# Kernel optimization log

Hardware: AMD Instinct MI355X
Metric: run time of the kernel (lower is better)

The kernel has to match this reference:

```python
import jax, jax.numpy as jnp
import numpy as np

D_MODEL = 1024
N_HEADS = 16
SEQ = 2048
BATCH = 2


def setup_inputs() -> dict:
    key = jax.random.key(0)
    ks = jax.random.split(key, 12)
    s = 1.0 / np.sqrt(D_MODEL)
    return {
        "q_input": jax.random.normal(ks[0], (BATCH, SEQ, D_MODEL), jnp.float32),
        "k_input": jax.random.normal(ks[1], (BATCH, SEQ, D_MODEL), jnp.float32),
        "v_input": jax.random.normal(ks[2], (BATCH, SEQ, D_MODEL), jnp.float32),
        "key_padding_mask": jnp.zeros((BATCH, SEQ), dtype=bool),
        "wq": jax.random.normal(ks[3], (D_MODEL, D_MODEL), jnp.float32) * s,
        "bq": jnp.zeros((D_MODEL,), jnp.float32),
        "wk": jax.random.normal(ks[4], (D_MODEL, D_MODEL), jnp.float32) * s,
        "bk": jnp.zeros((D_MODEL,), jnp.float32),
        "wv": jax.random.normal(ks[5], (D_MODEL, D_MODEL), jnp.float32) * s,
        "bv": jnp.zeros((D_MODEL,), jnp.float32),
        "wo": jax.random.normal(ks[6], (D_MODEL, D_MODEL), jnp.float32) * s,
        "bo": jnp.zeros((D_MODEL,), jnp.float32),
    }


def reference(q_input, k_input, v_input, key_padding_mask, wq, bq, wk, bk, wv, bv, wo, bo):
    B, Lq, _ = q_input.shape
    Lk = k_input.shape[1]
    d_head = D_MODEL // N_HEADS
    # torch Linear: x @ W.T + b
    Q = q_input @ wq.T + bq
    K = k_input @ wk.T + bk
    V = v_input @ wv.T + bv
    # [B, H, L, d_head]
    Qh = Q.reshape(B, Lq, N_HEADS, d_head).transpose(0, 2, 1, 3)
    Kh = K.reshape(B, Lk, N_HEADS, d_head).transpose(0, 2, 1, 3)
    Vh = V.reshape(B, Lk, N_HEADS, d_head).transpose(0, 2, 1, 3)
    scores = jnp.einsum("bhqd,bhkd->bhqk", Qh, Kh) / jnp.sqrt(jnp.float32(d_head))
    # causal mask (use_mask=True)
    causal = jnp.arange(Lk)[None, :] > jnp.arange(Lq)[:, None]  # [Lq, Lk]
    scores = jnp.where(causal[None, None], -jnp.inf, scores)
    # key padding mask [B,1,1,Lk]
    scores = jnp.where(key_padding_mask[:, None, None, :], -jnp.inf, scores)
    # module's global all-inf fallback (scalar condition)
    probs = jnp.where(
        jnp.all(jnp.isinf(scores)),
        jnp.full_like(scores, 1.0 / Lk),
        jax.nn.softmax(scores, axis=-1),
    )
    # dropout is identity in eval mode
    out = jnp.einsum("bhqk,bhkd->bhqd", probs, Vh)
    out = out.transpose(0, 2, 1, 3).reshape(B, Lq, D_MODEL)
    return out @ wo.T + bo
```

## Files before the change

### kernel.cpp

```cpp
#include <hip/hip_runtime.h>
#include <cstdint>
#include <cstddef>

#define DM   1024
#define HEADS 16
#define DH    64
#define SEQL  2048
#define BATCH 2
#define MTOT  (BATCH*SEQL)

typedef __attribute__((ext_vector_type(8))) short short8;
typedef __attribute__((ext_vector_type(4))) float floatx4;

__device__ __forceinline__ unsigned short f2bf(float f) {
  unsigned int u = __float_as_uint(f);
  u = (u + 0x7FFFu + ((u >> 16) & 1u)) >> 16;
  return (unsigned short)u;
}

__device__ __forceinline__ float exp2_fast(float x) {
#if __has_builtin(__builtin_amdgcn_exp2f)
  return __builtin_amdgcn_exp2f(x);
#else
  return exp2f(x);
#endif
}

__device__ __forceinline__ unsigned int cvt_pk_bf16(float lo, float hi) {
  unsigned int r;
  asm("v_cvt_pk_bf16_f32 %0, %1, %2" : "=v"(r) : "v"(lo), "v"(hi));
  return r;
}

__device__ __forceinline__ void async_ld16(const void* g, void* l) {
  __builtin_amdgcn_global_load_lds(
      (const __attribute__((address_space(1))) unsigned int*)g,
      (__attribute__((address_space(3))) unsigned int*)l, 16, 0, 0);
}

#define QSCALE 0.1803368801111204f

__global__ void cvt_all(const float* __restrict__ q, const float* __restrict__ k,
                        const float* __restrict__ v, const float* __restrict__ w0,
                        const float* __restrict__ w1, const float* __restrict__ w2,
                        const float* __restrict__ w3,
                        unsigned short* __restrict__ Xq, unsigned short* __restrict__ Xk,
                        unsigned short* __restrict__ Xv, unsigned short* __restrict__ W0,
                        unsigned short* __restrict__ W1, unsigned short* __restrict__ W2,
                        unsigned short* __restrict__ W3) {
  const int bid = blockIdx.x;
  const float* src; unsigned short* dst; int base;
  if (bid < 12288) {
    int seg = bid >> 12;
    base = (bid & 4095) * 1024;
    src = seg == 0 ? q : seg == 1 ? k : v;
    dst = seg == 0 ? Xq : seg == 1 ? Xk : Xv;
  } else {
    int b2 = bid - 12288;
    int seg = b2 >> 10;
    base = (b2 & 1023) * 1024;
    src = seg == 0 ? w0 : seg == 1 ? w1 : seg == 2 ? w2 : w3;
    dst = seg == 0 ? W0 : seg == 1 ? W1 : seg == 2 ? W2 : W3;
  }
  int i = base + threadIdx.x * 4;
  float4 vv = *(const float4*)(src + i);
  ushort4 o;
  o.x = f2bf(vv.x); o.y = f2bf(vv.y); o.z = f2bf(vv.z); o.w = f2bf(vv.w);
  *(ushort4*)(dst + i) = o;
}

__global__ __launch_bounds__(256, 3) void qkv_gemm(
    const unsigned short* Xq, const unsigned short* Xk, const unsigned short* Xv,
    const unsigned short* Wq, const unsigned short* Wk, const unsigned short* Wv,
    const float* bq, const float* bk, const float* bv,
    unsigned short* Qo, unsigned short* Ko, unsigned short* VTo) {
  __shared__ unsigned short As[128 * 64], Bs[128 * 64];
  const unsigned short *A, *Bw; const float* bias; unsigned short* Cout;
  if (blockIdx.z == 0)      { A = Xq; Bw = Wq; bias = bq; Cout = Qo; }
  else if (blockIdx.z == 1) { A = Xk; Bw = Wk; bias = bk; Cout = Ko; }
  else                      { A = Xv; Bw = Wv; bias = bv; Cout = VTo; }

  const int K = DM, N = DM;
  const int m0 = blockIdx.y * 128, n0 = blockIdx.x * 128;
  const int tid  = threadIdx.x;
  const int lane = tid & 63, wvi = tid >> 6;
  const int lq = lane & 15, quad = lane >> 4;
  const int wrow = wvi >> 1, wcol = wvi & 1;

  floatx4 acc[4][4];
  #pragma unroll
  for (int i = 0; i < 4; i++)
    #pragma unroll
    for (int j = 0; j < 4; j++)
      #pragma unroll
      for (int e = 0; e < 4; e++) acc[i][j][e] = 0.0f;

  for (int kt = 0; kt < K; kt += 64) {
    #pragma unroll
    for (int cc = 0; cc < 4; cc++) {
      int c = wvi + cc * 4;
      int e = c * 512 + lane * 8;
      int r = e >> 6, col = e & 63;
      async_ld16(A  + (size_t)(m0 + r) * K + kt + col, As + c * 512);
      async_ld16(Bw + (size_t)(n0 + r) * K + kt + col, Bs + c * 512);
    }
    __syncthreads();
    #pragma unroll
    for (int ks = 0; ks < 64; ks += 32) {
      short8 af[4], bf[4];
      #pragma unroll
      for (int i = 0; i < 4; i++)
        af[i] = *(const short8*)&As[(wrow * 64 + i * 16 + lq) * 64 + ks + quad * 8];
      #pragma unroll
      for (int j = 0; j < 4; j++)
        bf[j] = *(const short8*)&Bs[(wcol * 64 + j * 16 + lq) * 64 + ks + quad * 8];
      #pragma unroll
      for (int i = 0; i < 4; i++)
        #pragma unroll
        for (int j = 0; j < 4; j++)
          acc[i][j] = __builtin_amdgcn_mfma_f32_16x16x32_bf16(af[i], bf[j], acc[i][j], 0, 0, 0);
    }
    __syncthreads();
  }

  if (blockIdx.z == 2) {
    #pragma unroll
    for (int i = 0; i < 4; i++) {
      const int rowg = m0 + wrow * 64 + i * 16 + quad * 4;
      const int bb  = rowg >> 11;
      const int kt2 = (rowg & 2047) >> 6;
      const int k0  = rowg & 63;
      #pragma unroll
      for (int j = 0; j < 4; j++) {
        const int colg = n0 + wcol * 64 + j * 16 + lq;
        const int h2 = colg >> 6, d2 = colg & 63;
        const float bb_v = bias[colg];
        ushort4 w;
        w.x = f2bf(acc[i][j][0] + bb_v);
        w.y = f2bf(acc[i][j][1] + bb_v);
        w.z = f2bf(acc[i][j][2] + bb_v);
        w.w = f2bf(acc[i][j][3] + bb_v);
        *(ushort4*)(Cout + (size_t)((bb * HEADS + h2) * 32 + kt2) * 4096 + d2 * 64 + k0) = w;
      }
    }
  } else {
    const float oscale = (blockIdx.z == 0) ? QSCALE : 1.0f;
    #pragma unroll
    for (int i = 0; i < 4; i++) {
      #pragma unroll
      for (int j = 0; j < 4; j++) {
        int colg = n0 + wcol * 64 + j * 16 + lq;
        float bb = bias[colg];
        #pragma unroll
        for (int r = 0; r < 4; r++) {
          int rowg = m0 + wrow * 64 + i * 16 + quad * 4 + r;
          Cout[(size_t)rowg * N + colg] = f2bf((acc[i][j][r] + bb) * oscale);
        }
      }
    }
  }
}

__global__ __launch_bounds__(256, 4) void out_gemm(
    const unsigned short* __restrict__ A, const unsigned short* __restrict__ Bw,
    const float* __restrict__ bias, float* __restrict__ C) {
  __shared__ unsigned short As[64 * 64], Bs[128 * 64];
  const int K = DM, N = DM;
  const int m0 = blockIdx.y * 64, n0 = blockIdx.x * 128;
  const int tid  = threadIdx.x;
  const int lane = tid & 63, wvi = tid >> 6;
  const int lq = lane & 15, quad = lane >> 4;

  floatx4 acc[8];
  #pragma unroll
  for (int j = 0; j < 8; j++)
    #pragma unroll
    for (int e = 0; e < 4; e++) acc[j][e] = 0.0f;

  for (int kt = 0; kt < K; kt += 64) {
    #pragma unroll
    for (int cc = 0; cc < 2; cc++) {
      int c = wvi + cc * 4;
      int e = c * 512 + lane * 8;
      int r = e >> 6, col = e & 63;
      async_ld16(A + (size_t)(m0 + r) * K + kt + col, As + c * 512);
    }
    #pragma unroll
    for (int cc = 0; cc < 4; cc++) {
      int c = wvi + cc * 4;
      int e = c * 512 + lane * 8;
      int r = e >> 6, col = e & 63;
      async_ld16(Bw + (size_t)(n0 + r) * K + kt + col, Bs + c * 512);
    }
    __syncthreads();
    #pragma unroll
    for (int ks = 0; ks < 64; ks += 32) {
      const short8 af = *(const short8*)&As[(wvi * 16 + lq) * 64 + ks + quad * 8];
      #pragma unroll
      for (int j = 0; j < 8; j++) {
        const short8 bf = *(const short8*)&Bs[(j * 16 + lq) * 64 + ks + quad * 8];
        acc[j] = __builtin_amdgcn_mfma_f32_16x16x32_bf16(af, bf, acc[j], 0, 0, 0);
      }
    }
    __syncthreads();
  }

  #pragma unroll
  for (int j = 0; j < 8; j++) {
    const int colg = n0 + j * 16 + lq;
    const float bb = bias[colg];
    #pragma unroll
    for (int r = 0; r < 4; r++) {
      const int rowg = m0 + wvi * 16 + quad * 4 + r;
      C[(size_t)rowg * N + colg] = acc[j][r] + bb;
    }
  }
}

__global__ __launch_bounds__(256, 2) void attn_kernel(
    const unsigned short* __restrict__ Q, const unsigned short* __restrict__ K,
    const unsigned short* __restrict__ VT, const unsigned char* __restrict__ kpm,
    unsigned short* __restrict__ O) {
  __shared__ unsigned short Ks[64 * 72];
  __shared__ unsigned short VTs[64 * 72];
  __shared__ unsigned short Ps[4][2][16 * 72];

  const int bid = blockIdx.x;
  const int qt = 15 - (bid >> 5);
  const int bh = bid & 31;
  const int h = bh & 15, b = bh >> 4;
  const int tid = threadIdx.x, lane = tid & 63, wvi = tid >> 6;
  const int lq = lane & 15, quad = lane >> 4;
  const size_t bbase = (size_t)b * SEQL * DM;

  const int srow = tid >> 4;
  const int scol = (tid & 15) * 4;

  const unsigned short* kptr = K + bbase + (size_t)h * DH + (size_t)srow * DM + scol;
  const unsigned short* vptr = VT + (size_t)(b * HEADS + h) * 32 * 4096 + srow * 64 + scol;
  const unsigned char*  mptr = kpm + (size_t)b * SEQL + quad * 4;

  short8 qf[2][2];
  #pragma unroll
  for (int g = 0; g < 2; g++) {
    const unsigned short* Qrow =
        Q + bbase + (size_t)(qt * 128 + g * 64 + wvi * 16 + lq) * DM + h * DH;
    qf[g][0] = *(const short8*)(Qrow + quad * 8);
    qf[g][1] = *(const short8*)(Qrow + 32 + quad * 8);
  }

  ushort4 kr[4], vr[4];
  unsigned int mr[4];
  #pragma unroll
  for (int j = 0; j < 4; j++) {
    kr[j] = *(const ushort4*)(kptr + (size_t)j * 16 * DM);
    vr[j] = *(const ushort4*)(vptr + j * 1024);
  }
  #pragma unroll
  for (int t = 0; t < 4; t++) mr[t] = *(const unsigned int*)(mptr + t * 16);
  kptr += (size_t)64 * DM; vptr += 4096; mptr += 64;

  floatx4 o[2][4];
  floatx4 lacc[2];
  #pragma unroll
  for (int g = 0; g < 2; g++) {
    #pragma unroll
    for (int t = 0; t < 4; t++)
      #pragma unroll
      for (int e = 0; e < 4; e++) o[g][t][e] = 0.f;
    #pragma unroll
    for (int e = 0; e < 4; e++) lacc[g][e] = 0.f;
  }

  floatx4 zf;
  #pragma unroll
  for (int e = 0; e < 4; e++) zf[e] = 0.f;

  short8 ones8;
  #pragma unroll
  for (int e = 0; e < 8; e++) ones8[e] = (short)0x3F80;

  const int qg = wvi * 16 + lq;

  auto tile_body = [&](int m0, int m1, const unsigned int* mcur) {
    floatx4 st[2][4];
    #pragma unroll
    for (int t = 0; t < 4; t++) {
      const short8 a0 = *(const short8*)&Ks[(t * 16 + lq) * 72 + quad * 8];
      const short8 a1 = *(const short8*)&Ks[(t * 16 + lq) * 72 + 32 + quad * 8];
      if (m0 != 2) {
        st[0][t] = __builtin_amdgcn_mfma_f32_16x16x32_bf16(a0, qf[0][0], zf, 0, 0, 0);
        st[0][t] = __builtin_amdgcn_mfma_f32_16x16x32_bf16(a1, qf[0][1], st[0][t], 0, 0, 0);
      }
      st[1][t] = __builtin_amdgcn_mfma_f32_16x16x32_bf16(a0, qf[1][0], zf, 0, 0, 0);
      st[1][t] = __builtin_amdgcn_mfma_f32_16x16x32_bf16(a1, qf[1][1], st[1][t], 0, 0, 0);
    }

    const bool any_pad =
        __any((int)((mcur[0] | mcur[1] | mcur[2] | mcur[3]) != 0u));

    #pragma unroll
    for (int g = 0; g < 2; g++) {
      if (g == 0 && m0 == 2) continue;
      const int dmode = (g == 0) ? m0 : m1;
      float x[4][4];
      #pragma unroll
      for (int t = 0; t < 4; t++)
        #pragma unroll
        for (int r = 0; r < 4; r++) x[t][r] = st[g][t][r];

      if (any_pad) {
        #pragma unroll
        for (int t = 0; t < 4; t++)
          #pragma unroll
          for (int r = 0; r < 4; r++)
            if ((mcur[t] >> (8 * r)) & 0xffu) x[t][r] = -1e33f;
      }
      if (dmode == 1) {
        #pragma unroll
        for (int t = 0; t < 4; t++)
          #pragma unroll
          for (int r = 0; r < 4; r++)
            if (t * 16 + quad * 4 + r > qg) x[t][r] = -1e33f;
      }

      #pragma unroll
      for (int t = 0; t < 4; t++)
        #pragma unroll
        for (int r = 0; r < 4; r++)
          x[t][r] = exp2_fast(x[t][r]);

      #pragma unroll
      for (int t = 0; t < 4; t++) {
        unsigned int p01 = cvt_pk_bf16(x[t][0], x[t][1]);
        unsigned int p23 = cvt_pk_bf16(x[t][2], x[t][3]);
        *(uint2*)&Ps[wvi][g][lq * 72 + t * 16 + quad * 4] = make_uint2(p01, p23);
      }
    }

    short8 pa[2][2];
    if (m0 != 2) {
      pa[0][0] = *(const short8*)&Ps[wvi][0][lq * 72 + quad * 8];
      pa[0][1] = *(const short8*)&Ps[wvi][0][lq * 72 + 32 + quad * 8];
    }
    pa[1][0] = *(const short8*)&Ps[wvi][1][lq * 72 + quad * 8];
    pa[1][1] = *(const short8*)&Ps[wvi][1][lq * 72 + 32 + quad * 8];

    #pragma unroll
    for (int t = 0; t < 4; t++) {
      const short8 b0 = *(const short8*)&VTs[(t * 16 + lq) * 72 + quad * 8];
      const short8 b1 = *(const short8*)&VTs[(t * 16 + lq) * 72 + 32 + quad * 8];
      if (m0 != 2) {
        o[0][t] = __builtin_amdgcn_mfma_f32_16x16x32_bf16(pa[0][0], b0, o[0][t], 0, 0, 0);
        o[0][t] = __builtin_amdgcn_mfma_f32_16x16x32_bf16(pa[0][1], b1, o[0][t], 0, 0, 0);
      }
      o[1][t] = __builtin_amdgcn_mfma_f32_16x16x32_bf16(pa[1][0], b0, o[1][t], 0, 0, 0);
      o[1][t] = __builtin_amdgcn_mfma_f32_16x16x32_bf16(pa[1][1], b1, o[1][t], 0, 0, 0);
    }
    if (m0 != 2) {
      lacc[0] = __builtin_amdgcn_mfma_f32_16x16x32_bf16(pa[0][0], ones8, lacc[0], 0, 0, 0);
      lacc[0] = __builtin_amdgcn_mfma_f32_16x16x32_bf16(pa[0][1], ones8, lacc[0], 0, 0, 0);
    }
    lacc[1] = __builtin_amdgcn_mfma_f32_16x16x32_bf16(pa[1][0], ones8, lacc[1], 0, 0, 0);
    lacc[1] = __builtin_amdgcn_mfma_f32_16x16x32_bf16(pa[1][1], ones8, lacc[1], 0, 0, 0);
  };

  const int nkt = 2 * qt + 2;
  for (int kt = 0; kt < nkt - 1; kt++) {
    __syncthreads();
    #pragma unroll
    for (int j = 0; j < 4; j++) {
      *(ushort4*)&Ks [(j * 16 + srow) * 72 + scol] = kr[j];
      *(ushort4*)&VTs[(j * 16 + srow) * 72 + scol] = vr[j];
    }
    unsigned int mcur[4];
    #pragma unroll
    for (int t = 0; t < 4; t++) mcur[t] = mr[t];
    __syncthreads();

    #pragma unroll
    for (int j = 0; j < 4; j++) {
      kr[j] = *(const ushort4*)(kptr + (size_t)j * 16 * DM);
      vr[j] = *(const ushort4*)(vptr + j * 1024);
    }
    #pragma unroll
    for (int t = 0; t < 4; t++) mr[t] = *(const unsigned int*)(mptr + t * 16);
    kptr += (size_t)64 * DM; vptr += 4096; mptr += 64;

    tile_body(kt == nkt - 2 ? 1 : 0, 0, mcur);
  }

  __syncthreads();
  #pragma unroll
  for (int j = 0; j < 4; j++) {
    *(ushort4*)&Ks [(j * 16 + srow) * 72 + scol] = kr[j];
    *(ushort4*)&VTs[(j * 16 + srow) * 72 + scol] = vr[j];
  }
  __syncthreads();
  tile_body(2, 1, mr);

  #pragma unroll
  for (int g = 0; g < 2; g++) {
    float linv[4];
    #pragma unroll
    for (int r = 0; r < 4; r++) linv[r] = 1.0f / lacc[g][r];
    #pragma unroll
    for (int t = 0; t < 4; t++)
      #pragma unroll
      for (int r = 0; r < 4; r++) {
        const int rowg = qt * 128 + g * 64 + wvi * 16 + quad * 4 + r;
        const int colg = h * 64 + t * 16 + lq;
        O[bbase + (size_t)rowg * DM + colg] = f2bf(o[g][t][r] * linv[r]);
      }
  }
}

extern "C" void kernel_launch(void* const* d_in, const int* in_sizes, int n_in,
                              void* d_out, int out_size, void* d_ws, size_t ws_size,
                              hipStream_t stream) {
  const float* qin = (const float*)d_in[0];
  const float* kin = (const float*)d_in[1];
  const float* vin = (const float*)d_in[2];
  const unsigned char* kpm = (const unsigned char*)d_in[3];
  const float* wq = (const float*)d_in[4];
  const float* bq = (const float*)d_in[5];
  const float* wk = (const float*)d_in[6];
  const float* bk = (const float*)d_in[7];
  const float* wv = (const float*)d_in[8];
  const float* bv = (const float*)d_in[9];
  const float* wo = (const float*)d_in[10];
  const float* bo = (const float*)d_in[11];

  const size_t XN = (size_t)MTOT * DM;
  const size_t WN = (size_t)DM * DM;
  unsigned short* Xq  = (unsigned short*)d_ws;
  unsigned short* Xk  = Xq  + XN;
  unsigned short* Xv  = Xk  + XN;
  unsigned short* Wqb = Xv  + XN;
  unsigned short* Wkb = Wqb + WN;
  unsigned short* Wvb = Wkb + WN;
  unsigned short* Wob = Wvb + WN;
  unsigned short* Qb  = Wob + WN;
  unsigned short* Kb  = Qb  + XN;
  unsigned short* VTg = Kb  + XN;
  unsigned short* Ob  = VTg + XN;

  cvt_all<<<dim3(16384), 256, 0, stream>>>(qin, kin, vin, wq, wk, wv, wo,
                                           Xq, Xk, Xv, Wqb, Wkb, Wvb, Wob);

  dim3 g1(DM / 128, MTOT / 128, 3);
  qkv_gemm<<<g1, 256, 0, stream>>>(Xq, Xk, Xv, Wqb, Wkb, Wvb, bq, bk, bv, Qb, Kb, VTg);

  attn_kernel<<<dim3(BATCH * HEADS * (SEQL / 128)), 256, 0, stream>>>(Qb, Kb, VTg, kpm, Ob);

  dim3 g2(DM / 128, MTOT / 64, 1);
  out_gemm<<<g2, 256, 0, stream>>>(Ob, Wob, bo, (float*)d_out);
}
```

Baseline: 222.8 us.

## Split attention into single-wave blocks loading K/V fragments directly from global

Each 256-thread attention block becomes four independent 64-thread blocks, one wave each, so there are 2048 blocks in total. Each wave loads K and V^T MFMA fragments straight from global memory (L2) into registers, double-buffering K across tiles. This drops the shared-memory staging of K/V and the two block barriers per tile. Block IDs are remapped so the heads sharing K/V land on the same XCD for L2 reuse. The cost is four times as much redundant global/L2 traffic for K/V, since the waves no longer share a staged tile, and it adds more register pressure.

Measured after the change: 255.6 us. +14.7%, slower.

```diff
diff --git a/kernel.cpp b/kernel.cpp
--- a/kernel.cpp
+++ b/kernel.cpp
@@ -217,49 +217,36 @@
   }
 }
 
-__global__ __launch_bounds__(256, 2) void attn_kernel(
+__global__ __launch_bounds__(64, 2) void attn_kernel(
     const unsigned short* __restrict__ Q, const unsigned short* __restrict__ K,
     const unsigned short* __restrict__ VT, const unsigned char* __restrict__ kpm,
     unsigned short* __restrict__ O) {
-  __shared__ unsigned short Ks[64 * 72];
-  __shared__ unsigned short VTs[64 * 72];
-  __shared__ unsigned short Ps[4][2][16 * 72];
+  __shared__ unsigned short Ps[2][16 * 72];
 
   const int bid = blockIdx.x;
-  const int qt = 15 - (bid >> 5);
-  const int bh = bid & 31;
+  const int xcd = bid & 7;
+  const int k2  = bid >> 3;
+  const int bh  = xcd * 4 + (k2 & 3);
+  const int ws  = (k2 >> 2) & 3;
+  const int qt  = 15 - (k2 >> 4);
   const int h = bh & 15, b = bh >> 4;
-  const int tid = threadIdx.x, lane = tid & 63, wvi = tid >> 6;
-  const int lq = lane & 15, quad = lane >> 4;
+  const int tid = threadIdx.x;
+  const int lq = tid & 15, quad = (tid >> 4) & 3;
   const size_t bbase = (size_t)b * SEQL * DM;
 
-  const int srow = tid >> 4;
-  const int scol = (tid & 15) * 4;
-
-  const unsigned short* kptr = K + bbase + (size_t)h * DH + (size_t)srow * DM + scol;
-  const unsigned short* vptr = VT + (size_t)(b * HEADS + h) * 32 * 4096 + srow * 64 + scol;
-  const unsigned char*  mptr = kpm + (size_t)b * SEQL + quad * 4;
+  const unsigned short* kbase = K + bbase + (size_t)lq * DM + h * DH + quad * 8;
+  const unsigned short* vbase = VT + (size_t)(b * HEADS + h) * 32 * 4096 + lq * 64 + quad * 8;
+  const unsigned char*  mbase = kpm + (size_t)b * SEQL + quad * 4;
 
   short8 qf[2][2];
   #pragma unroll
   for (int g = 0; g < 2; g++) {
     const unsigned short* Qrow =
-        Q + bbase + (size_t)(qt * 128 + g * 64 + wvi * 16 + lq) * DM + h * DH;
+        Q + bbase + (size_t)(qt * 128 + g * 64 + ws * 16 + lq) * DM + h * DH;
     qf[g][0] = *(const short8*)(Qrow + quad * 8);
     qf[g][1] = *(const short8*)(Qrow + 32 + quad * 8);
   }
 
-  ushort4 kr[4], vr[4];
-  unsigned int mr[4];
-  #pragma unroll
-  for (int j = 0; j < 4; j++) {
-    kr[j] = *(const ushort4*)(kptr + (size_t)j * 16 * DM);
-    vr[j] = *(const ushort4*)(vptr + j * 1024);
-  }
-  #pragma unroll
-  for (int t = 0; t < 4; t++) mr[t] = *(const unsigned int*)(mptr + t * 16);
-  kptr += (size_t)64 * DM; vptr += 4096; mptr += 64;
-
   floatx4 o[2][4];
   floatx4 lacc[2];
   #pragma unroll
@@ -280,20 +267,41 @@
   #pragma unroll
   for (int e = 0; e < 8; e++) ones8[e] = (short)0x3F80;
 
-  const int qg = wvi * 16 + lq;
-
-  auto tile_body = [&](int m0, int m1, const unsigned int* mcur) {
+  const int qg  = ws * 16 + lq;
+  const int nkt = 2 * qt + 2;
+
+  auto loadK = [&](short8 (&kf)[4][2], int kt) {
+    #pragma unroll
+    for (int t = 0; t < 4; t++) {
+      kf[t][0] = *(const short8*)(kbase + (size_t)(kt * 64 + t * 16) * DM);
+      kf[t][1] = *(const short8*)(kbase + (size_t)(kt * 64 + t * 16) * DM + 32);
+    }
+  };
+
+  auto body = [&](short8 (&kf)[4][2], int kt) {
+    short8 vf[4][2];
+    #pragma unroll
+    for (int t = 0; t < 4; t++) {
+      vf[t][0] = *(const short8*)(vbase + (size_t)kt * 4096 + t * 1024);
+      vf[t][1] = *(const short8*)(vbase + (size_t)kt * 4096 + t * 1024 + 32);
+    }
+    unsigned int mcur[4];
+    #pragma unroll
+    for (int t = 0; t < 4; t++)
+      mcur[t] = *(const unsigned int*)(mbase + kt * 64 + t * 16);
+
+    const int m0 = (kt == nkt - 2) ? 1 : (kt == nkt - 1 ? 2 : 0);
+    const int m1 = (kt == nkt - 1) ? 1 : 0;
+
     floatx4 st[2][4];
     #pragma unroll
     for (int t = 0; t < 4; t++) {
-      const short8 a0 = *(const short8*)&Ks[(t * 16 + lq) * 72 + quad * 8];
-      const short8 a1 = *(const short8*)&Ks[(t * 16 + lq) * 72 + 32 + quad * 8];
       if (m0 != 2) {
-        st[0][t] = __builtin_amdgcn_mfma_f32_16x16x32_bf16(a0, qf[0][0], zf, 0, 0, 0);
-        st[0][t] = __builtin_amdgcn_mfma_f32_16x16x32_bf16(a1, qf[0][1], st[0][t], 0, 0, 0);
-      }
-      st[1][t] = __builtin_amdgcn_mfma_f32_16x16x32_bf16(a0, qf[1][0], zf, 0, 0, 0);
-      st[1][t] = __builtin_amdgcn_mfma_f32_16x16x32_bf16(a1, qf[1][1], st[1][t], 0, 0, 0);
+        st[0][t] = __builtin_amdgcn_mfma_f32_16x16x32_bf16(kf[t][0], qf[0][0], zf, 0, 0, 0);
+        st[0][t] = __builtin_amdgcn_mfma_f32_16x16x32_bf16(kf[t][1], qf[0][1], st[0][t], 0, 0, 0);
+      }
+      st[1][t] = __builtin_amdgcn_mfma_f32_16x16x32_bf16(kf[t][0], qf[1][0], zf, 0, 0, 0);
+      st[1][t] = __builtin_amdgcn_mfma_f32_16x16x32_bf16(kf[t][1], qf[1][1], st[1][t], 0, 0, 0);
     }
 
     const bool any_pad =
@@ -334,28 +342,26 @@
       for (int t = 0; t < 4; t++) {
         unsigned int p01 = cvt_pk_bf16(x[t][0], x[t][1]);
         unsigned int p23 = cvt_pk_bf16(x[t][2], x[t][3]);
-        *(uint2*)&Ps[wvi][g][lq * 72 + t * 16 + quad * 4] = make_uint2(p01, p23);
+        *(uint2*)&Ps[g][lq * 72 + t * 16 + quad * 4] = make_uint2(p01, p23);
       }
     }
 
     short8 pa[2][2];
     if (m0 != 2) {
-      pa[0][0] = *(const short8*)&Ps[wvi][0][lq * 72 + quad * 8];
-      pa[0][1] = *(const short8*)&Ps[wvi][0][lq * 72 + 32 + quad * 8];
-    }
-    pa[1][0] = *(const short8*)&Ps[wvi][1][lq * 72 + quad * 8];
-    pa[1][1] = *(const short8*)&Ps[wvi][1][lq * 72 + 32 + quad * 8];
+      pa[0][0] = *(const short8*)&Ps[0][lq * 72 + quad * 8];
+      pa[0][1] = *(const short8*)&Ps[0][lq * 72 + 32 + quad * 8];
+    }
+    pa[1][0] = *(const short8*)&Ps[1][lq * 72 + quad * 8];
+    pa[1][1] = *(const short8*)&Ps[1][lq * 72 + 32 + quad * 8];
 
     #pragma unroll
     for (int t = 0; t < 4; t++) {
-      const short8 b0 = *(const short8*)&VTs[(t * 16 + lq) * 72 + quad * 8];
-      const short8 b1 = *(const short8*)&VTs[(t * 16 + lq) * 72 + 32 + quad * 8];
       if (m0 != 2) {
-        o[0][t] = __builtin_amdgcn_mfma_f32_16x16x32_bf16(pa[0][0], b0, o[0][t], 0, 0, 0);
-        o[0][t] = __builtin_amdgcn_mfma_f32_16x16x32_bf16(pa[0][1], b1, o[0][t], 0, 0, 0);
-      }
-      o[1][t] = __builtin_amdgcn_mfma_f32_16x16x32_bf16(pa[1][0], b0, o[1][t], 0, 0, 0);
-      o[1][t] = __builtin_amdgcn_mfma_f32_16x16x32_bf16(pa[1][1], b1, o[1][t], 0, 0, 0);
+        o[0][t] = __builtin_amdgcn_mfma_f32_16x16x32_bf16(pa[0][0], vf[t][0], o[0][t], 0, 0, 0);
+        o[0][t] = __builtin_amdgcn_mfma_f32_16x16x32_bf16(pa[0][1], vf[t][1], o[0][t], 0, 0, 0);
+      }
+      o[1][t] = __builtin_amdgcn_mfma_f32_16x16x32_bf16(pa[1][0], vf[t][0], o[1][t], 0, 0, 0);
+      o[1][t] = __builtin_amdgcn_mfma_f32_16x16x32_bf16(pa[1][1], vf[t][1], o[1][t], 0, 0, 0);
     }
     if (m0 != 2) {
       lacc[0] = __builtin_amdgcn_mfma_f32_16x16x32_bf16(pa[0][0], ones8, lacc[0], 0, 0, 0);
@@ -365,39 +371,14 @@
     lacc[1] = __builtin_amdgcn_mfma_f32_16x16x32_bf16(pa[1][1], ones8, lacc[1], 0, 0, 0);
   };
 
-  const int nkt = 2 * qt + 2;
-  for (int kt = 0; kt < nkt - 1; kt++) {
-    __syncthreads();
-    #pragma unroll
-    for (int j = 0; j < 4; j++) {
-      *(ushort4*)&Ks [(j * 16 + srow) * 72 + scol] = kr[j];
-      *(ushort4*)&VTs[(j * 16 + srow) * 72 + scol] = vr[j];
-    }
-    unsigned int mcur[4];
-    #pragma unroll
-    for (int t = 0; t < 4; t++) mcur[t] = mr[t];
-    __syncthreads();
-
-    #pragma unroll
-    for (int j = 0; j < 4; j++) {
-      kr[j] = *(const ushort4*)(kptr + (size_t)j * 16 * DM);
-      vr[j] = *(const ushort4*)(vptr + j * 1024);
-    }
-    #pragma unroll
-    for (int t = 0; t < 4; t++) mr[t] = *(const unsigned int*)(mptr + t * 16);
-    kptr += (size_t)64 * DM; vptr += 4096; mptr += 64;
-
-    tile_body(kt == nkt - 2 ? 1 : 0, 0, mcur);
-  }
-
-  __syncthreads();
-  #pragma unroll
-  for (int j = 0; j < 4; j++) {
-    *(ushort4*)&Ks [(j * 16 + srow) * 72 + scol] = kr[j];
-    *(ushort4*)&VTs[(j * 16 + srow) * 72 + scol] = vr[j];
-  }
-  __syncthreads();
-  tile_body(2, 1, mr);
+  short8 kA[4][2], kB[4][2];
+  loadK(kA, 0);
+  for (int kt = 0; kt < nkt; kt += 2) {
+    loadK(kB, kt + 1);
+    body(kA, kt);
+    if (kt + 2 < nkt) loadK(kA, kt + 2);
+    body(kB, kt + 1);
+  }
 
   #pragma unroll
   for (int g = 0; g < 2; g++) {
@@ -408,7 +389,7 @@
     for (int t = 0; t < 4; t++)
       #pragma unroll
       for (int r = 0; r < 4; r++) {
-        const int rowg = qt * 128 + g * 64 + wvi * 16 + quad * 4 + r;
+        const int rowg = qt * 128 + g * 64 + ws * 16 + quad * 4 + r;
         const int colg = h * 64 + t * 16 + lq;
         O[bbase + (size_t)rowg * DM + colg] = f2bf(o[g][t][r] * linv[r]);
       }
@@ -451,7 +432,7 @@
   dim3 g1(DM / 128, MTOT / 128, 3);
   qkv_gemm<<<g1, 256, 0, stream>>>(Xq, Xk, Xv, Wqb, Wkb, Wvb, bq, bk, bv, Qb, Kb, VTg);
 
-  attn_kernel<<<dim3(BATCH * HEADS * (SEQL / 128)), 256, 0, stream>>>(Qb, Kb, VTg, kpm, Ob);
+  attn_kernel<<<dim3(2048), 64, 0, stream>>>(Qb, Kb, VTg, kpm, Ob);
 
   dim3 g2(DM / 128, MTOT / 64, 1);
   out_gemm<<<g2, 256, 0, stream>>>(Ob, Wob, bo, (float*)d_out);
```
